# Performance work log

Measured on AMD Instinct MI355X. Metric: run time of the kernel, lower is better.

## Reference

```python
import jax, jax.numpy as jnp
import numpy as np

B, C, H, W = 64, 128, 56, 56
ALPHA = 0.001


def _build_inhi_mat(out_channels):
    # Circulant 0/1 band: row i has ones at columns (i-r//2 ... i+r//2) mod C,
    # exactly matching the torch double loop with modular wrap-around.
    r = out_channels // 8 + 1  # inhiRange
    i = np.arange(out_channels)[:, None]
    d = np.arange(-(r // 2), r // 2 + 1)[None, :]
    cols = (i + d) % out_channels  # [C, r]
    m = np.zeros((out_channels, out_channels), dtype=np.float32)
    m[np.repeat(i, d.shape[1], axis=1), cols] = 1.0
    return m


def setup_inputs() -> dict:
    key = jax.random.key(0)
    x = jax.random.normal(key, (B, C, H, W), dtype=jnp.float32)
    inhiMat = jnp.asarray(_build_inhi_mat(C))  # [C, C] constant buffer
    return {"x": x, "inhiMat": inhiMat}


def reference(x, inhiMat):
    b, c, h, w = x.shape
    inhiRange = c // 8 + 1
    # y = detach(x)^2 -> banded cross-channel sum (bmm with broadcast [C,C] mat)
    y = jax.lax.stop_gradient(x) ** 2
    y = y.reshape(b, c, h * w)
    y = jnp.einsum('ij,bjs->bis', inhiMat, y)  # same math as bmm with tiled inhi
    y = y.reshape(b, c, h, w)
    denom = (y * ALPHA / inhiRange + 1.0) ** 0.75
    return x / denom
```

## Files before the change

### kernel.cpp

```cpp
#include <hip/hip_runtime.h>


#define B_DIM 64
#define C_DIM 128
#define HW_DIM (56 * 56)
#define HW2 (HW_DIM / 2)
#define NCOL2 (B_DIM * HW2)
#define NSEG 2
#define SEGC (C_DIM / NSEG)
#define RING 17

__device__ __forceinline__ float pow_m075(float t) {
    return __builtin_amdgcn_exp2f(-0.75f * __builtin_amdgcn_logf(t));
}

__global__ __launch_bounds__(64) void lrn_kernel(const float2* __restrict__ x,
                                                 float2* __restrict__ out) {
    const float kAlphaOverR = 0.001f / 17.0f;

    const int col = blockIdx.x * 64 + threadIdx.x;
    const int b   = col / HW2;
    const int hw2 = col - b * HW2;
    const int c0  = blockIdx.y * SEGC;

    const float2* base = x + ((size_t)b * C_DIM) * HW2 + hw2;
    float2* obase      = out + ((size_t)b * C_DIM) * HW2 + hw2;

    float2 r[RING];
#pragma unroll
    for (int d = 0; d < RING; ++d) {
        const int ch = (c0 + d - 8 + C_DIM) & (C_DIM - 1);
        r[d] = base[(size_t)ch * HW2];
    }
    float sx = 0.f, sy = 0.f;
#pragma unroll
    for (int d = 0; d < RING; ++d) {
        sx += r[d].x * r[d].x;
        sy += r[d].y * r[d].y;
    }

#pragma unroll
    for (int i = 0; i < SEGC; ++i) {
        const int c = c0 + i;
        const int slot_out = i % RING;
        const int slot_x   = (i + 8) % RING;
        const int ch_in    = (c + 9) & (C_DIM - 1);

        const float2 vin = base[(size_t)ch_in * HW2];

        const float2 xc = r[slot_x];
        float2 o;
        o.x = xc.x * pow_m075(fmaf(sx, kAlphaOverR, 1.0f));
        o.y = xc.y * pow_m075(fmaf(sy, kAlphaOverR, 1.0f));
        obase[(size_t)c * HW2] = o;

        const float2 vout = r[slot_out];
        sx += vin.x * vin.x - vout.x * vout.x;
        sy += vin.y * vin.y - vout.y * vout.y;
        r[slot_out] = vin;
    }
}

extern "C" void kernel_launch(void* const* d_in, const int* in_sizes, int n_in,
                              void* d_out, int out_size, void* d_ws, size_t ws_size,
                              hipStream_t stream) {
    const float2* x = (const float2*)d_in[0];
    float2* out = (float2*)d_out;

    dim3 grid(NCOL2 / 64, NSEG);
    lrn_kernel<<<grid, 64, 0, stream>>>(x, out);
}
```

Baseline: 186.5 us.

## Use float4 columns and short 8-channel segments with all planes preloaded

Each thread now processes four spatial elements as float4 and covers only 8 output channels. It loads all 24 needed channel planes up front instead of streaming a 17-entry ring over 64 channels. This greatly increases grid parallelism and memory-level parallelism per thread. In exchange the halo reads grow, so each input plane is fetched about three times and redundant traffic must be absorbed by cache.

```diff
diff --git a/kernel.cpp b/kernel.cpp
--- a/kernel.cpp
+++ b/kernel.cpp
@@ -4,69 +4,70 @@
 #define B_DIM 64
 #define C_DIM 128
 #define HW_DIM (56 * 56)
-#define HW2 (HW_DIM / 2)
-#define NCOL2 (B_DIM * HW2)
-#define NSEG 2
-#define SEGC (C_DIM / NSEG)
-#define RING 17
+#define HW4 (HW_DIM / 4)
+#define NCOL4 (B_DIM * HW4)
+#define CH 8
+#define PLANES (CH + 16)
 
 __device__ __forceinline__ float pow_m075(float t) {
     return __builtin_amdgcn_exp2f(-0.75f * __builtin_amdgcn_logf(t));
 }
 
-__global__ __launch_bounds__(64) void lrn_kernel(const float2* __restrict__ x,
-                                                 float2* __restrict__ out) {
+__global__ __launch_bounds__(64, 4) void lrn_kernel(const float4* __restrict__ x,
+                                                    float4* __restrict__ out) {
     const float kAlphaOverR = 0.001f / 17.0f;
 
-    const int col = blockIdx.x * 64 + threadIdx.x;
-    const int b   = col / HW2;
-    const int hw2 = col - b * HW2;
-    const int c0  = blockIdx.y * SEGC;
+    const int col4 = blockIdx.x * 64 + threadIdx.x;
+    const int b    = col4 / HW4;
+    const int hw4  = col4 - b * HW4;
+    const int c0   = blockIdx.y * CH;
 
-    const float2* base = x + ((size_t)b * C_DIM) * HW2 + hw2;
-    float2* obase      = out + ((size_t)b * C_DIM) * HW2 + hw2;
+    const float4* base = x + ((size_t)b * C_DIM) * HW4 + hw4;
+    float4* obase      = out + ((size_t)b * C_DIM) * HW4 + hw4;
 
-    float2 r[RING];
+    float4 v[PLANES];
 #pragma unroll
-    for (int d = 0; d < RING; ++d) {
-        const int ch = (c0 + d - 8 + C_DIM) & (C_DIM - 1);
-        r[d] = base[(size_t)ch * HW2];
+    for (int j = 0; j < PLANES; ++j) {
+        const int ch = (c0 + j - 8 + C_DIM) & (C_DIM - 1);
+        v[j] = base[(size_t)ch * HW4];
     }
-    float sx = 0.f, sy = 0.f;
+
+    float sx = 0.f, sy = 0.f, sz = 0.f, sw = 0.f;
 #pragma unroll
-    for (int d = 0; d < RING; ++d) {
-        sx += r[d].x * r[d].x;
-        sy += r[d].y * r[d].y;
+    for (int j = 0; j < 17; ++j) {
+        sx = fmaf(v[j].x, v[j].x, sx);
+        sy = fmaf(v[j].y, v[j].y, sy);
+        sz = fmaf(v[j].z, v[j].z, sz);
+        sw = fmaf(v[j].w, v[j].w, sw);
     }
 
 #pragma unroll
-    for (int i = 0; i < SEGC; ++i) {
-        const int c = c0 + i;
-        const int slot_out = i % RING;
-        const int slot_x   = (i + 8) % RING;
-        const int ch_in    = (c + 9) & (C_DIM - 1);
-
-        const float2 vin = base[(size_t)ch_in * HW2];
-
-        const float2 xc = r[slot_x];
-        float2 o;
+    for (int i = 0; i < CH; ++i) {
+        const float4 xc = v[8 + i];
+        float4 o;
         o.x = xc.x * pow_m075(fmaf(sx, kAlphaOverR, 1.0f));
         o.y = xc.y * pow_m075(fmaf(sy, kAlphaOverR, 1.0f));
-        obase[(size_t)c * HW2] = o;
+        o.z = xc.z * pow_m075(fmaf(sz, kAlphaOverR, 1.0f));
+        o.w = xc.w * pow_m075(fmaf(sw, kAlphaOverR, 1.0f));
+        obase[(size_t)(c0 + i) * HW4] = o;
 
-        const float2 vout = r[slot_out];
-        sx += vin.x * vin.x - vout.x * vout.x;
-        sy += vin.y * vin.y - vout.y * vout.y;
-        r[slot_out] = vin;
+        if (i < CH - 1) {
+            const float4 a = v[17 + i];
+            const float4 d = v[i];
+            sx += a.x * a.x - d.x * d.x;
+            sy += a.y * a.y - d.y * d.y;
+            sz += a.z * a.z - d.z * d.z;
+            sw += a.w * a.w - d.w * d.w;
+        }
     }
 }
 
 extern "C" void kernel_launch(void* const* d_in, const int* in_sizes, int n_in,
                               void* d_out, int out_size, void* d_ws, size_t ws_size,
                               hipStream_t stream) {
-    const float2* x = (const float2*)d_in[0];
-    float2* out = (float2*)d_out;
+    const float4* x = (const float4*)d_in[0];
+    float4* out = (float4*)d_out;
 
-    dim3 grid(NCOL2 / 64, NSEG);
+    dim3 grid(NCOL4 / 64, C_DIM / CH);
     lrn_kernel<<<grid, 64, 0, stream>>>(x, out);
 }
```

Measured after the change: 187.3 us. No clear change (+0.4%).

## Preload all segment channel planes up front and split channels into four segments

Applied to the files above, without the earlier changes.

Each thread now loads every input plane its channel segment needs (segment plus 16 halo channels) into registers before any compute, separated by a scheduling barrier. The interleaved per-iteration loads through a ring buffer go away. Channels are split into four segments instead of two, which doubles the grid in y, and launch bounds request 3 waves per SIMD. This exposes all loads at once for memory-level parallelism, at the cost of more halo re-reads (16 extra planes per 32 instead of per 64) and higher register use.

```diff
diff --git a/kernel.cpp b/kernel.cpp
--- a/kernel.cpp
+++ b/kernel.cpp
@@ -6,16 +6,16 @@
 #define HW_DIM (56 * 56)
 #define HW2 (HW_DIM / 2)
 #define NCOL2 (B_DIM * HW2)
-#define NSEG 2
+#define NSEG 4
 #define SEGC (C_DIM / NSEG)
-#define RING 17
+#define PLANES (SEGC + 16)
 
 __device__ __forceinline__ float pow_m075(float t) {
     return __builtin_amdgcn_exp2f(-0.75f * __builtin_amdgcn_logf(t));
 }
 
-__global__ __launch_bounds__(64) void lrn_kernel(const float2* __restrict__ x,
-                                                 float2* __restrict__ out) {
+__global__ __launch_bounds__(64, 3) void lrn_kernel(const float2* __restrict__ x,
+                                                    float2* __restrict__ out) {
     const float kAlphaOverR = 0.001f / 17.0f;
 
     const int col = blockIdx.x * 64 + threadIdx.x;
@@ -26,38 +26,35 @@
     const float2* base = x + ((size_t)b * C_DIM) * HW2 + hw2;
     float2* obase      = out + ((size_t)b * C_DIM) * HW2 + hw2;
 
-    float2 r[RING];
+    float2 v[PLANES];
 #pragma unroll
-    for (int d = 0; d < RING; ++d) {
-        const int ch = (c0 + d - 8 + C_DIM) & (C_DIM - 1);
-        r[d] = base[(size_t)ch * HW2];
+    for (int j = 0; j < PLANES; ++j) {
+        const int ch = (c0 + j - 8 + C_DIM) & (C_DIM - 1);
+        v[j] = base[(size_t)ch * HW2];
     }
+    __builtin_amdgcn_sched_barrier(0);
+
     float sx = 0.f, sy = 0.f;
 #pragma unroll
-    for (int d = 0; d < RING; ++d) {
-        sx += r[d].x * r[d].x;
-        sy += r[d].y * r[d].y;
+    for (int j = 0; j < 17; ++j) {
+        sx = fmaf(v[j].x, v[j].x, sx);
+        sy = fmaf(v[j].y, v[j].y, sy);
     }
 
 #pragma unroll
     for (int i = 0; i < SEGC; ++i) {
-        const int c = c0 + i;
-        const int slot_out = i % RING;
-        const int slot_x   = (i + 8) % RING;
-        const int ch_in    = (c + 9) & (C_DIM - 1);
-
-        const float2 vin = base[(size_t)ch_in * HW2];
-
-        const float2 xc = r[slot_x];
+        const float2 xc = v[8 + i];
         float2 o;
         o.x = xc.x * pow_m075(fmaf(sx, kAlphaOverR, 1.0f));
         o.y = xc.y * pow_m075(fmaf(sy, kAlphaOverR, 1.0f));
-        obase[(size_t)c * HW2] = o;
+        obase[(size_t)(c0 + i) * HW2] = o;
 
-        const float2 vout = r[slot_out];
-        sx += vin.x * vin.x - vout.x * vout.x;
-        sy += vin.y * vin.y - vout.y * vout.y;
-        r[slot_out] = vin;
+        if (i < SEGC - 1) {
+            const float2 a = v[17 + i];
+            const float2 d = v[i];
+            sx += a.x * a.x - d.x * d.x;
+            sy += a.y * a.y - d.y * d.y;
+        }
     }
 }
 
```

Measured after the change: 185.7 us. Within noise of the previous version (-0.4%).
